# Kernel optimization log

Measured on AMD Instinct MI355X. Metric: run time of the kernel, lower is better.

Reference implementation:

```python
import jax, jax.numpy as jnp
import numpy as np
from jax import lax

B, TIN, N, TOUT, C = 8, 168, 1500, 24, 16
EMB, ALPHA, BETA, TOPK, DEPTH = 16, 1.5, 0.2, 12, 2
KERNELS = (2, 3, 6, 7)


def setup_inputs() -> dict:
    key = jax.random.key(0)
    ks = jax.random.split(key, 32)
    def rn(k, shape, scale=0.1):
        return jax.random.normal(k, shape, jnp.float32) * scale
    inp = {"x": jax.random.normal(ks[0], (B, TIN, N, 1), jnp.float32)}
    inp["pw"], inp["pb"] = rn(ks[1], (C, 1)), rn(ks[2], (C,))
    branch = C // len(KERNELS)
    for i, k in enumerate(KERNELS):
        inp[f"tw{k}"] = rn(ks[3 + 2 * i], (branch, C, 1, k))
        inp[f"tb{k}"] = rn(ks[4 + 2 * i], (branch,))
    inp["e1"], inp["e2"] = rn(ks[11], (N, EMB), 1.0), rn(ks[12], (N, EMB), 1.0)
    inp["gw1"], inp["gb1"] = rn(ks[13], (EMB, EMB)), rn(ks[14], (EMB,))
    inp["gw2"], inp["gb2"] = rn(ks[15], (EMB, EMB)), rn(ks[16], (EMB,))
    inp["mw"], inp["mb"] = rn(ks[17], (C, (DEPTH + 1) * C)), rn(ks[18], (C,))
    inp["rw1"], inp["rb1"] = rn(ks[19], (C, C)), rn(ks[20], (C,))
    inp["rw2"], inp["rb2"] = rn(ks[21], (TOUT, C)), rn(ks[22], (TOUT,))
    return inp


def _conv1x1(h, w, b):
    # h: [B, Cin, N, T], w: [Cout, Cin], b: [Cout]
    return jnp.einsum('bint,oi->bont', h, w) + b[None, :, None, None]


def _forward(x, pw, pb, tw2, tb2, tw3, tb3, tw6, tb6, tw7, tb7,
             e1, e2, gw1, gb1, gw2, gb2, mw, mb, rw1, rb1, rw2, rb2):
    h = jnp.transpose(x, (0, 3, 2, 1))                      # [B,1,N,TIN]
    h = _conv1x1(h, pw, pb)                                 # [B,C,N,TIN]
    # dilated inception: branches with kernels (2,3,6,7), truncate to shortest
    tlen = TIN - max(KERNELS) + 1
    outs = []
    for w, b in ((tw2, tb2), (tw3, tb3), (tw6, tb6), (tw7, tb7)):
        o = lax.conv_general_dilated(h, w, (1, 1), 'VALID',
                                     dimension_numbers=('NCHW', 'OIHW', 'NCHW'))
        outs.append(o[..., -tlen:] + b[None, :, None, None])
    h = jax.nn.relu(jnp.concatenate(outs, axis=1))          # [B,C,N,tlen]
    # adaptive top-k graph learning
    m1 = jnp.tanh(ALPHA * (e1 @ gw1 + gb1))
    m2 = jnp.tanh(ALPHA * (e2 @ gw2 + gb2))
    a = jax.nn.relu(jnp.tanh(ALPHA * (m1 @ m2.T - m2 @ m1.T)))  # [N,N]
    _, idx = lax.top_k(a, TOPK)
    mask = jnp.zeros((N, N), jnp.float32).at[jnp.arange(N)[:, None], idx].set(1.0)
    adj = a * mask
    # mix-hop graph convolution with row-normalized (A + I)
    adj = adj + jnp.eye(N, dtype=jnp.float32)
    adj = adj / jnp.sum(adj, axis=1, keepdims=True)
    hin = h
    hops = [h]
    for _ in range(DEPTH):
        h = BETA * hin + (1.0 - BETA) * jnp.einsum('bcwt,vw->bcvt', h, adj)
        hops.append(h)
    ho = jnp.concatenate(hops, axis=1)                      # [B,(D+1)C,N,tlen]
    h = jax.nn.relu(_conv1x1(ho, mw, mb))                   # [B,C,N,tlen]
    # dropout -> identity at inference
    r = jax.nn.relu(_conv1x1(h, rw1, rb1))
    y = _conv1x1(r, rw2, rb2)                               # [B,TOUT,N,tlen]
    return jnp.mean(y, axis=-1)                             # [B,TOUT,N]


def reference(x, pw, pb, tw2, tb2, tw3, tb3, tw6, tb6, tw7, tb7,
              e1, e2, gw1, gb1, gw2, gb2, mw, mb, rw1, rb1, rw2, rb2):
    return _forward(x, pw, pb, tw2, tb2, tw3, tb3, tw6, tb6, tw7, tb7,
                    e1, e2, gw1, gb1, gw2, gb2, mw, mb, rw1, rb1, rw2, rb2)
```

## Files before the change

kernel.cpp:

```cpp
#include <hip/hip_runtime.h>

#define BB 8
#define TIN 168
#define NN 1500
#define TOUTC 24
#define TLEN 162
#define NG 32
#define NTH 1024
#define SN 2
#define TOPKK 12
#define NTILE 94
#define NPAD 1504

#define OFF_M1   0
#define OFF_M2   24000
#define OFF_M1T  48000
#define OFF_M2T  72000
#define OFF_EW   96000
#define OFF_EB   96112
#define OFF_ADJ  96128
#define OFF_FR   135128
#define OFF_S16  136664
#define OFF_PART 328664

typedef __attribute__((ext_vector_type(8))) _Float16 half8;
typedef __attribute__((ext_vector_type(2))) _Float16 half2v;
typedef __attribute__((ext_vector_type(4))) float v4f;

__device__ __forceinline__ unsigned int pk2(float lo, float hi) {
    return __builtin_bit_cast(unsigned int, __builtin_amdgcn_cvt_pkrtz(lo, hi));
}
__device__ __forceinline__ float h2lo(unsigned int u) {
    return (float)__builtin_bit_cast(half2v, u).x;
}
__device__ __forceinline__ float h2hi(unsigned int u) {
    return (float)__builtin_bit_cast(half2v, u).y;
}
__device__ __forceinline__ half2v as_h2(unsigned int u) { return __builtin_bit_cast(half2v, u); }
__device__ __forceinline__ unsigned int as_u(half2v h) { return __builtin_bit_cast(unsigned int, h); }
__device__ __forceinline__ half8 as_h8(uint4 u) { return __builtin_bit_cast(half8, u); }

__global__ __launch_bounds__(256) void prep_kernel(
    const float* __restrict__ e1, const float* __restrict__ e2,
    const float* __restrict__ gw1, const float* __restrict__ gb1,
    const float* __restrict__ gw2, const float* __restrict__ gb2,
    const float* __restrict__ pw, const float* __restrict__ pb,
    const float* __restrict__ tw2, const float* __restrict__ tb2,
    const float* __restrict__ tw3, const float* __restrict__ tb3,
    const float* __restrict__ tw6, const float* __restrict__ tb6,
    const float* __restrict__ tw7, const float* __restrict__ tb7,
    const float* __restrict__ mw, const float* __restrict__ rw1,
    float* __restrict__ ws)
{
    int n = blockIdx.x * blockDim.x + threadIdx.x;
    if (n < NN) {
        float a1[16], a2[16];
        #pragma unroll
        for (int o = 0; o < 16; ++o) { a1[o] = gb1[o]; a2[o] = gb2[o]; }
        #pragma unroll
        for (int i = 0; i < 16; ++i) {
            float u = e1[n*16+i], v = e2[n*16+i];
            #pragma unroll
            for (int o = 0; o < 16; ++o) {
                a1[o] += u * gw1[i*16+o];
                a2[o] += v * gw2[i*16+o];
            }
        }
        #pragma unroll
        for (int o = 0; o < 16; ++o) {
            float t1v = tanhf(1.5f*a1[o]);
            float t2v = tanhf(1.5f*a2[o]);
            ws[OFF_M1 + n*16+o] = t1v;
            ws[OFF_M2 + n*16+o] = t2v;
            ws[OFF_M1T + o*NN + n] = t1v;
            ws[OFF_M2T + o*NN + n] = t2v;
        }
    }
    if (blockIdx.x == 0 && threadIdx.x < 16) {
        int c = threadIdx.x;
        int br = c >> 2, oc = c & 3;
        const float* tw; const float* tb; int k;
        if (br == 0)      { tw = tw2; tb = tb2; k = 2; }
        else if (br == 1) { tw = tw3; tb = tb3; k = 3; }
        else if (br == 2) { tw = tw6; tb = tb6; k = 6; }
        else              { tw = tw7; tb = tb7; k = 7; }
        for (int d = 0; d < 7; ++d) ws[OFF_EW + c*7 + d] = 0.f;
        float ebv = tb[oc];
        for (int j = 0; j < k; ++j) {
            float s = 0.f, sb = 0.f;
            for (int ic = 0; ic < 16; ++ic) {
                float w = tw[(oc*16+ic)*k + j];
                s  += w * pw[ic];
                sb += w * pb[ic];
            }
            ws[OFF_EW + c*7 + (7-k+j)] = s;
            ebv += sb;
        }
        ws[OFF_EB + c] = ebv;
    }
    if (blockIdx.x == 1 && threadIdx.x < 64) {
        int lane = threadIdx.x;
        int m = lane & 15, qq = lane >> 4;
        unsigned short* frw = (unsigned short*)(ws + OFF_FR);
        for (int mat = 0; mat < 3; ++mat) {
            for (int j = 0; j < 8; ++j) {
                int k = qq*8 + j;
                float s;
                if (mat == 0) s = (k < 16) ? mw[m*48+k] + 0.2f*(mw[m*48+16+k] + mw[m*48+32+k])
                                           : 0.8f*mw[m*48+16+(k-16)] + 0.16f*mw[m*48+32+(k-16)];
                else if (mat == 1) s = (k < 16) ? 0.64f*mw[m*48+32+k] : 0.f;
                else               s = (k < 16) ? rw1[m*16+k] : 0.f;
                _Float16 hi = (_Float16)s;
                _Float16 lo = (_Float16)(s - (float)hi);
                frw[(mat*2+0)*512 + lane*8 + j] = __builtin_bit_cast(unsigned short, hi);
                frw[(mat*2+1)*512 + lane*8 + j] = __builtin_bit_cast(unsigned short, lo);
            }
        }
    }
}

__global__ __launch_bounds__(256) void graph_kernel(
    const float* __restrict__ m1, const float* __restrict__ m2,
    const float* __restrict__ m1T, const float* __restrict__ m2T,
    int2* __restrict__ adj)
{
    int v = blockIdx.x;
    int tid = threadIdx.x;
    __shared__ float wv4[4];
    __shared__ int   wi4[4];
    __shared__ int   bcast_i;
    __shared__ float m1v[16], m2v[16];
    if (tid < 16) { m1v[tid] = m1[v*16+tid]; m2v[tid] = m2[v*16+tid]; }
    __syncthreads();
    float sreg[6];
    #pragma unroll
    for (int u = 0; u < 6; ++u) {
        int j = tid + 256*u;
        float a = -1.f;
        if (j < NN) {
            float d = 0.f;
            #pragma unroll
            for (int i = 0; i < 16; ++i)
                d += m1v[i]*m2T[i*NN+j] - m2v[i]*m1T[i*NN+j];
            float t = tanhf(1.5f*d);
            a = t > 0.f ? t : 0.f;
        }
        sreg[u] = a;
    }
    float lb = -1.f; int li = NN;
    #pragma unroll
    for (int u = 0; u < 6; ++u) {
        int j = tid + 256*u;
        if (j < NN && sreg[u] > lb) { lb = sreg[u]; li = j; }
    }
    const int wid = tid >> 6;
    float kw[TOPKK]; int ki[TOPKK];
    #pragma unroll
    for (int it = 0; it < TOPKK; ++it) {
        float bv = lb; int bi = li;
        #pragma unroll
        for (int off = 32; off > 0; off >>= 1) {
            float ov = __shfl_down(bv, off);
            int   oi = __shfl_down(bi, off);
            if (ov > bv || (ov == bv && oi < bi)) { bv = ov; bi = oi; }
        }
        if ((tid & 63) == 0) { wv4[wid] = bv; wi4[wid] = bi; }
        __syncthreads();
        if (tid == 0) {
            #pragma unroll
            for (int w = 1; w < 4; ++w) {
                float ov = wv4[w]; int oi = wi4[w];
                if (ov > bv || (ov == bv && oi < bi)) { bv = ov; bi = oi; }
            }
            kw[it] = bv; ki[it] = bi;
            bcast_i = bi;
        }
        __syncthreads();
        int win = bcast_i;
        if (li == win) {
            #pragma unroll
            for (int u = 0; u < 6; ++u)
                if (tid + 256*u == win) sreg[u] = -1.f;
            lb = -1.f; li = NN;
            #pragma unroll
            for (int u = 0; u < 6; ++u) {
                int j = tid + 256*u;
                if (j < NN && sreg[u] > lb) { lb = sreg[u]; li = j; }
            }
        }
    }
    if (tid == 0) {
        float s = 1.f;
        #pragma unroll
        for (int it = 0; it < TOPKK; ++it) s += kw[it];
        float inv = 1.f/s;
        #pragma unroll
        for (int it = 0; it < TOPKK; ++it) {
            float w = kw[it]*inv;
            adj[it*NN + v] = make_int2((int)pk2(w, w), ki[it]);
        }
        adj[TOPKK*NN + v] = make_int2((int)pk2(inv, inv), v);
    }
}

__device__ __forceinline__ half8 ldfrag(const unsigned short* fr, int plane, int lane) {
    const uint4* p = (const uint4*)(fr + plane*512);
    return as_h8(p[lane]);
}

__global__ __launch_bounds__(NTH, 4) void main_kernel(
    const float* __restrict__ x,
    const float* __restrict__ ew, const float* __restrict__ eb,
    const int2* __restrict__ adj,
    const unsigned short* __restrict__ fr,
    unsigned int* __restrict__ part,
    const float* __restrict__ mb, const float* __restrict__ rb1)
{
    __shared__ uint4 feat[6][NPAD];

    const int tid = threadIdx.x;
    const int lane = tid & 63;
    const int wid = tid >> 6;
    const int b = blockIdx.x >> 5;
    const int g = blockIdx.x & 31;
    const int t0 = (g*TLEN) >> 5;
    const int t1 = ((g+1)*TLEN) >> 5;
    const int n0 = lane & 15, q = lane >> 4;
    unsigned int* partBG = part + (size_t)(b*NG + g)*NN*8;

    #pragma unroll 1
    for (int s = 0; s < SN; ++s) {
        int v = tid + NTH*s;
        if (v < NN) {
            float xv[7];
            #pragma unroll
            for (int d = 0; d < 7; ++d) xv[d] = x[(b*TIN + t0 + d)*NN + v];
            float h[16];
            #pragma unroll
            for (int c = 0; c < 16; ++c) {
                float a = eb[c];
                #pragma unroll
                for (int d = 0; d < 7; ++d) a += ew[c*7+d]*xv[d];
                h[c] = a > 0.f ? a : 0.f;
            }
            feat[0][v] = make_uint4(pk2(h[0],h[1]), pk2(h[2],h[3]), pk2(h[4],h[5]), pk2(h[6],h[7]));
            feat[1][v] = make_uint4(pk2(h[8],h[9]), pk2(h[10],h[11]), pk2(h[12],h[13]), pk2(h[14],h[15]));
        }
    }
    __syncthreads();

    for (int t = t0; t < t1; ++t) {
        const int par = (t - t0) & 1;
        const int hc = par ? 4 : 0;
        const int hn = par ? 0 : 4;

        #pragma unroll 1
        for (int s = 0; s < SN; ++s) {
            int v = tid + NTH*s;
            if (v < NN) {
                const half2v zero = {(_Float16)0.f, (_Float16)0.f};
                half2v acc[8];
                #pragma unroll
                for (int i = 0; i < 8; ++i) acc[i] = zero;
                #pragma unroll
                for (int j = 0; j < 13; ++j) {
                    int2 aw = adj[j*NN + v];
                    half2v w2 = as_h2((unsigned int)aw.x);
                    int nb = aw.y;
                    uint4 b0 = feat[hc][nb], b1 = feat[hc+1][nb];
                    acc[0] = as_h2(b0.x) * w2 + acc[0];
                    acc[1] = as_h2(b0.y) * w2 + acc[1];
                    acc[2] = as_h2(b0.z) * w2 + acc[2];
                    acc[3] = as_h2(b0.w) * w2 + acc[3];
                    acc[4] = as_h2(b1.x) * w2 + acc[4];
                    acc[5] = as_h2(b1.y) * w2 + acc[5];
                    acc[6] = as_h2(b1.z) * w2 + acc[6];
                    acc[7] = as_h2(b1.w) * w2 + acc[7];
                }
                feat[2][v] = make_uint4(as_u(acc[0]), as_u(acc[1]), as_u(acc[2]), as_u(acc[3]));
                feat[3][v] = make_uint4(as_u(acc[4]), as_u(acc[5]), as_u(acc[6]), as_u(acc[7]));
            }
        }
        __syncthreads();

        {
            half8 a1h = ldfrag(fr, 0, lane), a1l = ldfrag(fr, 1, lane);
            half8 a2h = ldfrag(fr, 2, lane), a2l = ldfrag(fr, 3, lane);
            uint2* zH = (uint2*)feat[hc + (q >> 1)];
            uint2* pH = (uint2*)feat[2  + (q >> 1)];
            #pragma unroll 1
            for (int T = wid; T < NTILE; T += 16) {
                int n = T*16 + n0;
                half8 bf  = as_h8(feat[(q < 2) ? (hc + q) : q][n]);
                half8 b2f = as_h8(feat[2 + (q & 1)][n]);
                v4f z = {0.f,0.f,0.f,0.f}, p = {0.f,0.f,0.f,0.f};
                z = __builtin_amdgcn_mfma_f32_16x16x32_f16(a1h, bf, z, 0, 0, 0);
                z = __builtin_amdgcn_mfma_f32_16x16x32_f16(a1l, bf, z, 0, 0, 0);
                p = __builtin_amdgcn_mfma_f32_16x16x32_f16(a2h, b2f, p, 0, 0, 0);
                p = __builtin_amdgcn_mfma_f32_16x16x32_f16(a2l, b2f, p, 0, 0, 0);
                uint2 zz; zz.x = pk2(z[0], z[1]); zz.y = pk2(z[2], z[3]);
                uint2 pp; pp.x = pk2(p[0], p[1]); pp.y = pk2(p[2], p[3]);
                zH[n*2 + (q & 1)] = zz;
                pH[n*2 + (q & 1)] = pp;
            }
        }
        __syncthreads();

        if (t + 1 < t1) {
            #pragma unroll 1
            for (int s = 0; s < SN; ++s) {
                int v = tid + NTH*s;
                if (v < NN) {
                    float xv[7];
                    #pragma unroll
                    for (int d = 0; d < 7; ++d) xv[d] = x[(b*TIN + (t+1) + d)*NN + v];
                    float h[16];
                    #pragma unroll
                    for (int c = 0; c < 16; ++c) {
                        float a = eb[c];
                        #pragma unroll
                        for (int d = 0; d < 7; ++d) a += ew[c*7+d]*xv[d];
                        h[c] = a > 0.f ? a : 0.f;
                    }
                    feat[hn][v]   = make_uint4(pk2(h[0],h[1]), pk2(h[2],h[3]), pk2(h[4],h[5]), pk2(h[6],h[7]));
                    feat[hn+1][v] = make_uint4(pk2(h[8],h[9]), pk2(h[10],h[11]), pk2(h[12],h[13]), pk2(h[14],h[15]));
                }
            }
        }
        {
            half8 a3h = ldfrag(fr, 4, lane), a3l = ldfrag(fr, 5, lane);
            float mbq[4], rbq[4];
            #pragma unroll
            for (int r = 0; r < 4; ++r) { mbq[r] = mb[q*4+r]; rbq[r] = rb1[q*4+r]; }
            uint2* zH = (uint2*)feat[hc + (q >> 1)];
            const uint2* pH = (const uint2*)feat[2 + (q >> 1)];
            #pragma unroll 1
            for (int T = wid; T < NTILE; T += 16) {
                int n = T*16 + n0;
                uint2 zz = zH[n*2 + (q & 1)];
                int vc = n < NN ? n : NN-1;
                const half2v zero = {(_Float16)0.f, (_Float16)0.f};
                half2v ga = zero, gb = zero;
                #pragma unroll
                for (int j = 0; j < 13; ++j) {
                    int2 aw = adj[j*NN + vc];
                    half2v w2 = as_h2((unsigned int)aw.x);
                    int nb = aw.y;
                    uint2 ps = pH[nb*2 + (q & 1)];
                    ga = as_h2(ps.x) * w2 + ga;
                    gb = as_h2(ps.y) * w2 + gb;
                }
                float y0 = mbq[0] + h2lo(zz.x) + (float)ga.x;
                float y1 = mbq[1] + h2hi(zz.x) + (float)ga.y;
                float y2 = mbq[2] + h2lo(zz.y) + (float)gb.x;
                float y3 = mbq[3] + h2hi(zz.y) + (float)gb.y;
                y0 = y0 > 0.f ? y0 : 0.f;  y1 = y1 > 0.f ? y1 : 0.f;
                y2 = y2 > 0.f ? y2 : 0.f;  y3 = y3 > 0.f ? y3 : 0.f;
                uint2 ypk; ypk.x = pk2(y0, y1); ypk.y = pk2(y2, y3);
                zH[n*2 + (q & 1)] = ypk;
                asm volatile("" ::: "memory");
                half8 bfY = as_h8(feat[(q < 2) ? (hc + q) : q][n]);
                v4f acc = {0.f,0.f,0.f,0.f};
                acc = __builtin_amdgcn_mfma_f32_16x16x32_f16(a3h, bfY, acc, 0, 0, 0);
                acc = __builtin_amdgcn_mfma_f32_16x16x32_f16(a3l, bfY, acc, 0, 0, 0);
                if (n < NN) {
                    float r0 = acc[0]+rbq[0], r1 = acc[1]+rbq[1], r2 = acc[2]+rbq[2], r3 = acc[3]+rbq[3];
                    r0 = r0 > 0.f ? r0 : 0.f;  r1 = r1 > 0.f ? r1 : 0.f;
                    r2 = r2 > 0.f ? r2 : 0.f;  r3 = r3 > 0.f ? r3 : 0.f;
                    uint2 nv; nv.x = pk2(r0, r1); nv.y = pk2(r2, r3);
                    uint2* pp = (uint2*)(partBG + (size_t)n*8 + q*2);
                    if (t == t0) {
                        *pp = nv;
                    } else {
                        uint2 o = *pp;
                        uint2 m;
                        m.x = as_u(as_h2(o.x) + as_h2(nv.x));
                        m.y = as_u(as_h2(o.y) + as_h2(nv.y));
                        *pp = m;
                    }
                }
            }
        }
        __syncthreads();
    }
}

__global__ __launch_bounds__(256) void reduce1_kernel(const unsigned int* __restrict__ part,
                                                      float* __restrict__ s16buf)
{
    int idx = blockIdx.x*256 + threadIdx.x;
    if (idx >= BB*NN*8) return;
    int cp = idx & 7;
    int rest = idx >> 3;
    float s0 = 0.f, s1 = 0.f;
    #pragma unroll
    for (int g = 0; g < NG; ++g) {
        int bb = rest / NN, vv = rest % NN;
        unsigned int u = part[((size_t)(bb*NG + g)*NN + vv)*8 + cp];
        s0 += h2lo(u); s1 += h2hi(u);
    }
    float2* o = (float2*)(s16buf + (size_t)rest*16 + cp*2);
    *o = make_float2(s0 * (1.0f/TLEN), s1 * (1.0f/TLEN));
}

__global__ __launch_bounds__(256) void reduce2_kernel(const float* __restrict__ s16buf,
                                                      const float* __restrict__ rw2,
                                                      const float* __restrict__ rb2,
                                                      float* __restrict__ out)
{
    int idx = blockIdx.x*256 + threadIdx.x;
    if (idx >= BB*NN) return;
    int v = idx % NN;
    int b = idx / NN;
    const float4* sp = (const float4*)(s16buf + (size_t)idx*16);
    float4 s0 = sp[0], s1 = sp[1], s2 = sp[2], s3 = sp[3];
    float s16[16] = {s0.x,s0.y,s0.z,s0.w, s1.x,s1.y,s1.z,s1.w,
                     s2.x,s2.y,s2.z,s2.w, s3.x,s3.y,s3.z,s3.w};
    #pragma unroll
    for (int o = 0; o < TOUTC; ++o) {
        float a = rb2[o];
        #pragma unroll
        for (int c = 0; c < 16; ++c) a += rw2[o*16+c]*s16[c];
        out[(b*TOUTC + o)*NN + v] = a;
    }
}

extern "C" void kernel_launch(void* const* d_in, const int* in_sizes, int n_in,
                              void* d_out, int out_size, void* d_ws, size_t ws_size,
                              hipStream_t stream)
{
    const float* x   = (const float*)d_in[0];
    const float* pw  = (const float*)d_in[1];
    const float* pb  = (const float*)d_in[2];
    const float* tw2 = (const float*)d_in[3];
    const float* tb2 = (const float*)d_in[4];
    const float* tw3 = (const float*)d_in[5];
    const float* tb3 = (const float*)d_in[6];
    const float* tw6 = (const float*)d_in[7];
    const float* tb6 = (const float*)d_in[8];
    const float* tw7 = (const float*)d_in[9];
    const float* tb7 = (const float*)d_in[10];
    const float* e1  = (const float*)d_in[11];
    const float* e2  = (const float*)d_in[12];
    const float* gw1 = (const float*)d_in[13];
    const float* gb1 = (const float*)d_in[14];
    const float* gw2 = (const float*)d_in[15];
    const float* gb2 = (const float*)d_in[16];
    const float* mw  = (const float*)d_in[17];
    const float* mb  = (const float*)d_in[18];
    const float* rw1 = (const float*)d_in[19];
    const float* rb1 = (const float*)d_in[20];
    const float* rw2 = (const float*)d_in[21];
    const float* rb2 = (const float*)d_in[22];
    float* ws  = (float*)d_ws;
    float* out = (float*)d_out;

    prep_kernel<<<(NN + 255)/256, 256, 0, stream>>>(e1,e2,gw1,gb1,gw2,gb2,pw,pb,
                                                    tw2,tb2,tw3,tb3,tw6,tb6,tw7,tb7,
                                                    mw, rw1, ws);
    graph_kernel<<<NN, 256, 0, stream>>>(ws + OFF_M1, ws + OFF_M2,
                                         ws + OFF_M1T, ws + OFF_M2T,
                                         (int2*)(ws + OFF_ADJ));
    main_kernel<<<BB*NG, NTH, 0, stream>>>(x, ws + OFF_EW, ws + OFF_EB,
                                           (const int2*)(ws + OFF_ADJ),
                                           (const unsigned short*)(ws + OFF_FR),
                                           (unsigned int*)(ws + OFF_PART), mb, rb1);
    reduce1_kernel<<<(BB*NN*8 + 255)/256, 256, 0, stream>>>((const unsigned int*)(ws + OFF_PART),
                                                            ws + OFF_S16);
    reduce2_kernel<<<(BB*NN + 255)/256, 256, 0, stream>>>(ws + OFF_S16, rw2, rb2, out);
}
```

Before: 292.7 us.

## Fuse partial reductions into one kernel and reorder adjacency entries for LDS banks

The two reduction kernels are merged into one, which drops the intermediate s16 buffer and one launch. Each thread now sums all 32 group partials for one (b,v) using 16-byte loads and applies the output projection directly. Separately, the graph kernel sorts each node's 13 neighbour entries by index mod 8 and rotates them by v mod 13. This is presumably meant to spread LDS bank accesses in the main kernel's neighbour gather. The merged reduction launches 8x fewer threads with more serial work each, which may cost parallelism.

```diff
diff --git a/kernel.cpp b/kernel.cpp
--- a/kernel.cpp
+++ b/kernel.cpp
@@ -20,7 +20,6 @@
 #define OFF_EB   96112
 #define OFF_ADJ  96128
 #define OFF_FR   135128
-#define OFF_S16  136664
 #define OFF_PART 328664
 
 typedef __attribute__((ext_vector_type(8))) _Float16 half8;
@@ -194,12 +193,21 @@
         #pragma unroll
         for (int it = 0; it < TOPKK; ++it) s += kw[it];
         float inv = 1.f/s;
-        #pragma unroll
-        for (int it = 0; it < TOPKK; ++it) {
-            float w = kw[it]*inv;
-            adj[it*NN + v] = make_int2((int)pk2(w, w), ki[it]);
-        }
-        adj[TOPKK*NN + v] = make_int2((int)pk2(inv, inv), v);
+        float w13[13]; int i13[13];
+        #pragma unroll
+        for (int it = 0; it < TOPKK; ++it) { w13[it] = kw[it]*inv; i13[it] = ki[it]; }
+        w13[12] = inv; i13[12] = v;
+        for (int a = 1; a < 13; ++a) {
+            float wv = w13[a]; int iv = i13[a]; int key = iv & 7;
+            int c = a - 1;
+            while (c >= 0 && (i13[c] & 7) > key) { w13[c+1] = w13[c]; i13[c+1] = i13[c]; --c; }
+            w13[c+1] = wv; i13[c+1] = iv;
+        }
+        int rot = v % 13;
+        for (int j = 0; j < 13; ++j) {
+            int sidx = j + rot; if (sidx >= 13) sidx -= 13;
+            adj[j*NN + v] = make_int2((int)pk2(w13[sidx], w13[sidx]), i13[sidx]);
+        }
     }
 }
 
@@ -385,42 +393,34 @@
     }
 }
 
-__global__ __launch_bounds__(256) void reduce1_kernel(const unsigned int* __restrict__ part,
-                                                      float* __restrict__ s16buf)
-{
-    int idx = blockIdx.x*256 + threadIdx.x;
-    if (idx >= BB*NN*8) return;
-    int cp = idx & 7;
-    int rest = idx >> 3;
-    float s0 = 0.f, s1 = 0.f;
-    #pragma unroll
-    for (int g = 0; g < NG; ++g) {
-        int bb = rest / NN, vv = rest % NN;
-        unsigned int u = part[((size_t)(bb*NG + g)*NN + vv)*8 + cp];
-        s0 += h2lo(u); s1 += h2hi(u);
-    }
-    float2* o = (float2*)(s16buf + (size_t)rest*16 + cp*2);
-    *o = make_float2(s0 * (1.0f/TLEN), s1 * (1.0f/TLEN));
-}
-
-__global__ __launch_bounds__(256) void reduce2_kernel(const float* __restrict__ s16buf,
-                                                      const float* __restrict__ rw2,
-                                                      const float* __restrict__ rb2,
-                                                      float* __restrict__ out)
+__global__ __launch_bounds__(256) void reduce_kernel(const unsigned int* __restrict__ part,
+                                                     const float* __restrict__ rw2,
+                                                     const float* __restrict__ rb2,
+                                                     float* __restrict__ out)
 {
     int idx = blockIdx.x*256 + threadIdx.x;
     if (idx >= BB*NN) return;
     int v = idx % NN;
     int b = idx / NN;
-    const float4* sp = (const float4*)(s16buf + (size_t)idx*16);
-    float4 s0 = sp[0], s1 = sp[1], s2 = sp[2], s3 = sp[3];
-    float s16[16] = {s0.x,s0.y,s0.z,s0.w, s1.x,s1.y,s1.z,s1.w,
-                     s2.x,s2.y,s2.z,s2.w, s3.x,s3.y,s3.z,s3.w};
+    float s[16];
+    #pragma unroll
+    for (int c = 0; c < 16; ++c) s[c] = 0.f;
+    #pragma unroll 4
+    for (int g = 0; g < NG; ++g) {
+        const uint4* p4 = (const uint4*)(part + ((size_t)(b*NG + g)*NN + v)*8);
+        uint4 u0 = p4[0], u1 = p4[1];
+        s[0] += h2lo(u0.x); s[1] += h2hi(u0.x); s[2]  += h2lo(u0.y); s[3]  += h2hi(u0.y);
+        s[4] += h2lo(u0.z); s[5] += h2hi(u0.z); s[6]  += h2lo(u0.w); s[7]  += h2hi(u0.w);
+        s[8] += h2lo(u1.x); s[9] += h2hi(u1.x); s[10] += h2lo(u1.y); s[11] += h2hi(u1.y);
+        s[12]+= h2lo(u1.z); s[13]+= h2hi(u1.z); s[14] += h2lo(u1.w); s[15] += h2hi(u1.w);
+    }
+    #pragma unroll
+    for (int c = 0; c < 16; ++c) s[c] *= (1.0f/TLEN);
     #pragma unroll
     for (int o = 0; o < TOUTC; ++o) {
         float a = rb2[o];
         #pragma unroll
-        for (int c = 0; c < 16; ++c) a += rw2[o*16+c]*s16[c];
+        for (int c = 0; c < 16; ++c) a += rw2[o*16+c]*s[c];
         out[(b*TOUTC + o)*NN + v] = a;
     }
 }
@@ -465,7 +465,6 @@
                                            (const int2*)(ws + OFF_ADJ),
                                            (const unsigned short*)(ws + OFF_FR),
                                            (unsigned int*)(ws + OFF_PART), mb, rb1);
-    reduce1_kernel<<<(BB*NN*8 + 255)/256, 256, 0, stream>>>((const unsigned int*)(ws + OFF_PART),
-                                                            ws + OFF_S16);
-    reduce2_kernel<<<(BB*NN + 255)/256, 256, 0, stream>>>(ws + OFF_S16, rw2, rb2, out);
-}
+    reduce_kernel<<<(BB*NN + 255)/256, 256, 0, stream>>>((const unsigned int*)(ws + OFF_PART),
+                                                         rw2, rb2, out);
+}
```

Result: no change. 298.1 us (+1.8%).
